# Optimization experiments

Measured on AMD Instinct MI355X. Metric: run time of the kernel, lower is better.

Reference implementation:

```python
import jax, jax.numpy as jnp
import numpy as np

GRID_SIZE = 5
SPLINE_ORDER = 3
TY = 16  # n_ahead


def b_splines(x, grid):
    # x: (B, in), grid: (in, grid_size + 2*spline_order + 1) -> (B, in, grid_size+spline_order)
    x = x[..., None]
    bases = ((x >= grid[:, :-1]) & (x < grid[:, 1:])).astype(x.dtype)
    for k in range(1, SPLINE_ORDER + 1):
        bases = ((x - grid[:, :-(k + 1)]) / (grid[:, k:-1] - grid[:, :-(k + 1)]) * bases[..., :-1]
                 + (grid[:, k + 1:] - x) / (grid[:, k + 1:] - grid[:, 1:-k]) * bases[..., 1:])
    return bases


def kan_linear(x, grid, base_weight, spline_weight, spline_scaler):
    # efficient-kan KANLinear: SiLU base branch + scaled spline branch
    base = jnp.dot(jax.nn.silu(x), base_weight.T)                  # (B, out)
    scaled_sw = spline_weight * spline_scaler[..., None]            # (out, in, coeff)
    spl = jnp.einsum('big,oig->bo', b_splines(x, grid), scaled_sw)
    return base + spl


def setup_inputs() -> dict:
    key = jax.random.key(0)
    ks = jax.random.split(key, 8)
    B, Tx, IN0, H, OUT = 1024, 64, 256, 512, 1
    coeff = GRID_SIZE + SPLINE_ORDER
    x = jax.random.normal(ks[0], (B, Tx, IN0), dtype=jnp.float32)
    h0 = jnp.zeros((B, H), dtype=jnp.float32)
    hstep = 2.0 / GRID_SIZE  # grid_range [-1, 1]
    grid1d = jnp.arange(-SPLINE_ORDER, GRID_SIZE + SPLINE_ORDER + 1, dtype=jnp.float32) * hstep - 1.0
    grid = jnp.broadcast_to(grid1d, (IN0, grid1d.shape[0])).astype(jnp.float32)
    base_weight = jax.random.normal(ks[1], (H, IN0), jnp.float32) * (1.0 / np.sqrt(IN0))
    spline_weight = jax.random.normal(ks[2], (H, IN0, coeff), jnp.float32) * 0.1
    spline_scaler = jax.random.normal(ks[3], (H, IN0), jnp.float32) * (1.0 / np.sqrt(IN0))
    h2h_w = jax.random.normal(ks[4], (H, H), jnp.float32) * (1.0 / np.sqrt(H))
    h2h_b = jnp.zeros((H,), jnp.float32)
    fc_w = jax.random.normal(ks[5], (OUT, H), jnp.float32) * (1.0 / np.sqrt(H))
    fc_b = jnp.zeros((OUT,), jnp.float32)
    return {"x": x, "h0": h0, "grid": grid, "base_weight": base_weight,
            "spline_weight": spline_weight, "spline_scaler": spline_scaler,
            "h2h_w": h2h_w, "h2h_b": h2h_b, "fc_w": fc_w, "fc_b": fc_b}


def reference(x, h0, grid, base_weight, spline_weight, spline_scaler, h2h_w, h2h_b, fc_w, fc_b):
    B, Tx, IN0 = x.shape

    def enc_step(h, x_t):
        h_new = jnp.tanh(kan_linear(x_t, grid, base_weight, spline_weight, spline_scaler)
                         + jnp.dot(h, h2h_w.T) + h2h_b)
        return h_new, h_new

    h_last, h_enc = jax.lax.scan(enc_step, h0, jnp.swapaxes(x, 0, 1))  # h_enc: (Tx, B, H)

    # decode steps are fed x = zeros, so the KAN input branch is a constant
    i2h_zero = kan_linear(jnp.zeros((B, IN0), x.dtype), grid, base_weight, spline_weight, spline_scaler)

    def dec_step(h, _):
        h_new = jnp.tanh(i2h_zero + jnp.dot(h, h2h_w.T) + h2h_b)
        return h_new, h_new

    _, h_dec = jax.lax.scan(dec_step, h_last, None, length=TY)  # (Ty, B, H)

    h_all = jnp.concatenate([jnp.swapaxes(h_enc, 0, 1), jnp.swapaxes(h_dec, 0, 1)], axis=1)  # (B, Tx+Ty, H)
    y = jnp.dot(h_dec, fc_w.T) + fc_b        # (Ty, B, 1)
    y_pred = jnp.swapaxes(y[..., 0], 0, 1)   # (B, Ty)  == y_pred.squeeze(dim=2)
    return (y_pred, h_all)
```

## Files before the change

kernel.cpp:

```cpp
#include <hip/hip_runtime.h>


using s16x8 = __attribute__((ext_vector_type(8))) short;
using u16x8 = __attribute__((ext_vector_type(8))) unsigned short;
using f32x4 = __attribute__((ext_vector_type(4))) float;
using u32x2 = __attribute__((ext_vector_type(2))) unsigned;

#define HALL_TSTRIDE 512
#define HALL_BSTRIDE (80 * 512)

__device__ __forceinline__ unsigned short f2bf(float f) {
  unsigned u = __builtin_bit_cast(unsigned, f);
  u += 0x7fffu + ((u >> 16) & 1u);
  return (unsigned short)(u >> 16);
}
__device__ __forceinline__ float bf2f(unsigned short h) {
  unsigned u = ((unsigned)h) << 16;
  return __builtin_bit_cast(float, u);
}
__device__ __forceinline__ float silu(float x) {
  return x / (1.f + __expf(-x));
}
__device__ __forceinline__ float tanh_fast(float x) {
  float e2 = __expf(2.f * x);
  return 1.f - 2.f * __builtin_amdgcn_rcpf(e2 + 1.f);
}

__device__ __forceinline__ void basis8_f32(float xv, float g0, float invh, float* out) {
  float u = (xv - g0) * invh;
  float fs = floorf(u);
  int s = (int)fs;
  float r = u - fs;
  float omr = 1.f - r;
  float r2 = r * r, r3 = r2 * r;
  float n0 = (1.f / 6.f) * omr * omr * omr;
  float n1 = (1.f / 6.f) * (3.f * r3 - 6.f * r2 + 4.f);
  float n2 = (1.f / 6.f) * (-3.f * r3 + 3.f * r2 + 3.f * r + 1.f);
  float n3 = (1.f / 6.f) * r3;
#pragma unroll
  for (int j = 0; j < 8; ++j) {
    int d = s - j;
    out[j] = (d == 0) ? n3 : (d == 1) ? n2 : (d == 2) ? n1 : (d == 3) ? n0 : 0.f;
  }
}

__device__ __forceinline__ u16x8 basis8_bf16(float xv, float g0, float invh) {
  float t[8];
  basis8_f32(xv, g0, invh, t);
  u16x8 o;
#pragma unroll
  for (int j = 0; j < 8; ++j) o[j] = f2bf(t[j]);
  return o;
}

__global__ __launch_bounds__(256) void prep_waug2(const float* __restrict__ bw,
                                                  const float* __restrict__ sw,
                                                  const float* __restrict__ sc,
                                                  unsigned short* __restrict__ Waug2) {
  int o = blockIdx.x;
  for (int k = threadIdx.x; k < 2304; k += 256) {
    float v;
    if (k < 256) {
      v = bw[o * 256 + k];
    } else {
      int idx = k - 256;
      int i = idx >> 3, g = idx & 7;
      v = sw[(o * 256 + i) * 8 + g] * sc[o * 256 + i];
    }
    int ks = k >> 6;
    int q = (k >> 3) & 7;
    int p = q ^ (o & 7);
    int e = k & 7;
    Waug2[(long)ks * 32768 + o * 64 + p * 8 + e] = f2bf(v);
  }
}

__global__ __launch_bounds__(256) void prep_whh(const float* __restrict__ w,
                                                unsigned short* __restrict__ hi,
                                                unsigned short* __restrict__ lo) {
  for (int i = blockIdx.x * 256 + threadIdx.x; i < 512 * 512; i += gridDim.x * 256) {
    float v = w[i];
    unsigned short h = f2bf(v);
    hi[i] = h;
    lo[i] = f2bf(v - bf2f(h));
  }
}

__global__ __launch_bounds__(256) void prep_i2hz(const float* __restrict__ sw,
                                                 const float* __restrict__ sc,
                                                 const float* __restrict__ grd,
                                                 float* __restrict__ i2hz,
                                                 unsigned* __restrict__ cnt) {
  __shared__ float red[256];
  const int o = blockIdx.x;
  const int t = threadIdx.x;
  if (o == 0) {
    for (int i = t; i < 64 * 32; i += 256) cnt[i] = 0u;
  }
  float g0 = grd[0];
  float invh = 1.f / (grd[1] - grd[0]);
  float bs[8];
  basis8_f32(0.f, g0, invh, bs);
  const float* swrow = sw + ((long)o * 256 + t) * 8;
  float a = 0.f;
#pragma unroll
  for (int j = 0; j < 8; ++j) a += bs[j] * swrow[j];
  red[t] = a * sc[o * 256 + t];
  __syncthreads();
  for (int w = 128; w > 0; w >>= 1) {
    if (t < w) red[t] += red[t + w];
    __syncthreads();
  }
  if (t == 0) i2hz[o] = red[0];
}

__global__ __launch_bounds__(512, 4) void kan_i2h_gemm(const float* __restrict__ x,
                                                       const float* __restrict__ grd,
                                                       const unsigned short* __restrict__ Waug2,
                                                       float* __restrict__ hall) {
  __shared__ __align__(128) short Bs[256 * 64];
  __shared__ __align__(128) short As[128 * 64];

  const int bid = blockIdx.x;
  const int m0 = (bid >> 1) * 128;
  const int n0 = (bid & 1) * 256;
  const int tid = threadIdx.x;
  const int lane = tid & 63, wave = tid >> 6;
  const int wr = wave >> 2, wc = wave & 3;
  const int colg = lane & 15, kgrp = lane >> 4;

  float g0 = grd[0];
  float invh = 1.f / (grd[1] - grd[0]);

  f32x4 acc[4][4] = {};

  const int arow = tid >> 2, apart = tid & 3;
  const float* xrow = x + (long)(m0 + arow) * 256;
  const int aswz = arow & 7;
  short* const adst0 = (short*)((char*)As + arow * 128 + ((apart * 2) ^ aswz) * 16);
  short* const adst1 = (short*)((char*)As + arow * 128 + ((apart * 2 + 1) ^ aswz) * 16);

  auto computeA = [&](int ks, u16x8& d0, u16x8& d1) {
    int kA = ks * 64 + apart * 16;
    if (ks < 4) {
      const float* xs = xrow + kA;
      f32x4 v0 = *(const f32x4*)(xs);
      f32x4 v1 = *(const f32x4*)(xs + 4);
      f32x4 v2 = *(const f32x4*)(xs + 8);
      f32x4 v3 = *(const f32x4*)(xs + 12);
#pragma unroll
      for (int e = 0; e < 4; ++e) {
        d0[e] = f2bf(silu(v0[e]));
        d0[e + 4] = f2bf(silu(v1[e]));
        d1[e] = f2bf(silu(v2[e]));
        d1[e + 4] = f2bf(silu(v3[e]));
      }
    } else {
      int i0 = (kA - 256) >> 3;
      d0 = basis8_bf16(xrow[i0], g0, invh);
      d1 = basis8_bf16(xrow[i0 + 1], g0, invh);
    }
  };

  u16x8 ar0, ar1;
  computeA(0, ar0, ar1);

  for (int ks = 0; ks < 36; ++ks) {
    {
      const char* bsrc = (const char*)Waug2 + (long)ks * 65536 + n0 * 128 +
                         wave * 4096 + lane * 16;
      char* bdst = (char*)Bs + wave * 4096;
#pragma unroll
      for (int i = 0; i < 4; ++i)
        __builtin_amdgcn_global_load_lds(
            (const __attribute__((address_space(1))) unsigned int*)(bsrc + i * 1024),
            (__attribute__((address_space(3))) unsigned int*)(bdst + i * 1024), 16, 0, 0);
    }
    *(u16x8*)adst0 = ar0;
    *(u16x8*)adst1 = ar1;
    __syncthreads();

    if (ks + 1 < 36) computeA(ks + 1, ar0, ar1);

#pragma unroll
    for (int kk = 0; kk < 2; ++kk) {
      const int q = kk * 4 + kgrp;
      s16x8 a[4], b[4];
#pragma unroll
      for (int i = 0; i < 4; ++i) {
        int ra = wr * 64 + i * 16 + colg;
        a[i] = *(const s16x8*)((const char*)As + ra * 128 + (q ^ (ra & 7)) * 16);
      }
#pragma unroll
      for (int j = 0; j < 4; ++j) {
        int rb = wc * 64 + j * 16 + colg;
        b[j] = *(const s16x8*)((const char*)Bs + rb * 128 + (q ^ (rb & 7)) * 16);
      }
#pragma unroll
      for (int i = 0; i < 4; ++i)
#pragma unroll
        for (int j = 0; j < 4; ++j)
          acc[i][j] = __builtin_amdgcn_mfma_f32_16x16x32_bf16(a[i], b[j], acc[i][j], 0, 0, 0);
    }
    __syncthreads();
  }

  const int c0 = n0 + wc * 64;
#pragma unroll
  for (int i = 0; i < 4; ++i) {
    int mbase = m0 + wr * 64 + i * 16 + (kgrp << 2);
#pragma unroll
    for (int r = 0; r < 4; ++r) {
      int m = mbase + r;
      int bb = m >> 6, tt = m & 63;
      float* orow = hall + (long)bb * HALL_BSTRIDE + (long)tt * HALL_TSTRIDE + c0;
#pragma unroll
      for (int j = 0; j < 4; ++j) orow[j * 16 + colg] = acc[i][j][r];
    }
  }
}

__device__ __forceinline__ void pack_write_h(f32x4 v, int rr, int c16,
                                             char* hHb, char* hLb) {
  unsigned h0 = f2bf(v[0]), h1 = f2bf(v[1]), h2 = f2bf(v[2]), h3 = f2bf(v[3]);
  unsigned l0 = f2bf(v[0] - bf2f((unsigned short)h0));
  unsigned l1 = f2bf(v[1] - bf2f((unsigned short)h1));
  unsigned l2 = f2bf(v[2] - bf2f((unsigned short)h2));
  unsigned l3 = f2bf(v[3] - bf2f((unsigned short)h3));
  u32x2 hw, lw;
  hw[0] = h0 | (h1 << 16); hw[1] = h2 | (h3 << 16);
  lw[0] = l0 | (l1 << 16); lw[1] = l2 | (l3 << 16);
  int byte = (rr * 1024 + c16 * 8) ^ ((rr & 7) << 4);
  *(u32x2*)(hHb + byte) = hw;
  *(u32x2*)(hLb + byte) = lw;
}

__global__ __launch_bounds__(512, 2) void rnn_persist(
    const unsigned short* __restrict__ WhhHi,
    const unsigned short* __restrict__ WhhLo,
    const float* __restrict__ i2hz,
    const float* __restrict__ h2hb,
    const float* __restrict__ h0,
    float* __restrict__ hall,
    unsigned* __restrict__ cnt) {
  __shared__ __align__(16) char hHb[16 * 1024];
  __shared__ __align__(16) char hLb[16 * 1024];

  const int tid = threadIdx.x;
  const int lane = tid & 63;
  const int wave = tid >> 6;
  const int bid = blockIdx.x;
  const int xcd = bid & 7;
  const int j = bid >> 3;
  const int cg = j & 3;
  const int g = xcd * 8 + (j >> 2);
  const int m0 = g * 16;
  const int colg = lane & 15;
  const int kgrp = lane >> 4;
  const int o = cg * 128 + wave * 16 + colg;
  const int aswz = (colg & 7) << 4;

  s16x8 wh[16], wl[16];
#pragma unroll
  for (int kk = 0; kk < 16; ++kk) {
    const unsigned short* ph = WhhHi + (long)o * 512 + kk * 32 + kgrp * 8;
    const unsigned short* pl = WhhLo + (long)o * 512 + kk * 32 + kgrp * 8;
    asm volatile("global_load_dwordx4 %0, %1, off" : "=v"(wh[kk]) : "v"(ph));
    asm volatile("global_load_dwordx4 %0, %1, off" : "=v"(wl[kk]) : "v"(pl));
  }
  const float bias = h2hb[o];
  const float i2z = i2hz[o];
  asm volatile("s_waitcnt vmcnt(0)" ::: "memory");
  __builtin_amdgcn_sched_barrier(0);

  {
    const int rr = tid >> 5, cc = tid & 31;
#pragma unroll
    for (int jj = 0; jj < 4; ++jj) {
      int c16 = cc + jj * 32;
      f32x4 v = *(const f32x4*)(h0 + (long)(m0 + rr) * 512 + c16 * 4);
      pack_write_h(v, rr, c16, hHb, hLb);
    }
  }
  __syncthreads();

  for (int T = 0; T < 80; ++T) {
    float i2v[4];
    if (T < 64) {
#pragma unroll
      for (int r = 0; r < 4; ++r) {
        const float* p = hall + (long)(m0 + kgrp * 4 + r) * HALL_BSTRIDE +
                         (long)T * HALL_TSTRIDE + o;
        asm volatile("global_load_dword %0, %1, off sc0 sc1" : "=v"(i2v[r]) : "v"(p));
      }
    }

    f32x4 aA = {}, aB = {}, aC = {};
#pragma unroll
    for (int kk = 0; kk < 16; ++kk) {
      int abyte = (colg * 1024 + kk * 64 + kgrp * 16) ^ aswz;
      s16x8 ah = *(const s16x8*)(hHb + abyte);
      s16x8 al = *(const s16x8*)(hLb + abyte);
      aA = __builtin_amdgcn_mfma_f32_16x16x32_bf16(ah, wh[kk], aA, 0, 0, 0);
      aB = __builtin_amdgcn_mfma_f32_16x16x32_bf16(ah, wl[kk], aB, 0, 0, 0);
      aC = __builtin_amdgcn_mfma_f32_16x16x32_bf16(al, wh[kk], aC, 0, 0, 0);
    }

    if (T < 64) {
      asm volatile("s_waitcnt vmcnt(0)" ::: "memory");
      __builtin_amdgcn_sched_barrier(0);
    } else {
#pragma unroll
      for (int r = 0; r < 4; ++r) i2v[r] = i2z;
    }

#pragma unroll
    for (int r = 0; r < 4; ++r) {
      float pre = aA[r] + aB[r] + aC[r] + i2v[r] + bias;
      float h = tanh_fast(pre);
      float* p = hall + (long)(m0 + kgrp * 4 + r) * HALL_BSTRIDE +
                 (long)T * HALL_TSTRIDE + o;
      asm volatile("global_store_dword %0, %1, off sc0 sc1" :: "v"(p), "v"(h) : "memory");
    }

    if (T == 79) break;

    asm volatile("s_waitcnt vmcnt(0)" ::: "memory");
    __syncthreads();
    if (tid == 0) {
      __hip_atomic_fetch_add(&cnt[g * 32], 1u, __ATOMIC_RELEASE,
                             __HIP_MEMORY_SCOPE_AGENT);
      unsigned tgt = 4u * (unsigned)(T + 1);
      while (__hip_atomic_load(&cnt[g * 32], __ATOMIC_RELAXED,
                               __HIP_MEMORY_SCOPE_AGENT) < tgt)
        __builtin_amdgcn_s_sleep(2);
    }
    __syncthreads();

    {
      const int rr = tid >> 5, cc = tid & 31;
      const float* src = hall + (long)(m0 + rr) * HALL_BSTRIDE + (long)T * HALL_TSTRIDE;
      f32x4 v[4];
#pragma unroll
      for (int jj = 0; jj < 4; ++jj) {
        const float* p = src + (cc + jj * 32) * 4;
        asm volatile("global_load_dwordx4 %0, %1, off sc0 sc1" : "=v"(v[jj]) : "v"(p));
      }
      asm volatile("s_waitcnt vmcnt(0)" ::: "memory");
      __builtin_amdgcn_sched_barrier(0);
#pragma unroll
      for (int jj = 0; jj < 4; ++jj) pack_write_h(v[jj], rr, cc + jj * 32, hHb, hLb);
    }
    __syncthreads();
  }
}

__global__ __launch_bounds__(256) void y_final(const float* __restrict__ hall,
                                               const float* __restrict__ fcw,
                                               const float* __restrict__ fcb,
                                               float* __restrict__ y) {
  int gw = (blockIdx.x * 256 + threadIdx.x) >> 6;
  int lane = threadIdx.x & 63;
  int bb = gw >> 4, ty = gw & 15;
  const float* hrow = hall + (long)bb * HALL_BSTRIDE + (long)(64 + ty) * HALL_TSTRIDE;
  float s = 0.f;
#pragma unroll
  for (int c = 0; c < 8; ++c) s += hrow[lane + c * 64] * fcw[lane + c * 64];
#pragma unroll
  for (int off = 32; off > 0; off >>= 1) s += __shfl_xor(s, off);
  if (lane == 0) y[bb * 16 + ty] = s + fcb[0];
}

extern "C" void kernel_launch(void* const* d_in, const int* in_sizes, int n_in,
                              void* d_out, int out_size, void* d_ws, size_t ws_size,
                              hipStream_t stream) {
  (void)in_sizes; (void)n_in; (void)out_size; (void)ws_size;
  const float* x   = (const float*)d_in[0];
  const float* h0  = (const float*)d_in[1];
  const float* grd = (const float*)d_in[2];
  const float* bw  = (const float*)d_in[3];
  const float* sw  = (const float*)d_in[4];
  const float* sc  = (const float*)d_in[5];
  const float* whh = (const float*)d_in[6];
  const float* hbb = (const float*)d_in[7];
  const float* fcw = (const float*)d_in[8];
  const float* fcb = (const float*)d_in[9];

  float* out = (float*)d_out;
  float* ypred = out;
  float* hall = out + 1024 * 16;

  char* ws = (char*)d_ws;
  unsigned short* Waug2 = (unsigned short*)(ws);
  unsigned short* WhhHi = (unsigned short*)(ws + 2359296);
  unsigned short* WhhLo = (unsigned short*)(ws + 2883584);
  float*          i2hz  = (float*)(ws + 3407872);
  unsigned*       cnt   = (unsigned*)(ws + 3409920);

  prep_waug2<<<512, 256, 0, stream>>>(bw, sw, sc, Waug2);
  prep_whh<<<512, 256, 0, stream>>>(whh, WhhHi, WhhLo);
  prep_i2hz<<<512, 256, 0, stream>>>(sw, sc, grd, i2hz, cnt);
  kan_i2h_gemm<<<1024, 512, 0, stream>>>(x, grd, Waug2, hall);
  rnn_persist<<<256, 512, 0, stream>>>(WhhHi, WhhLo, i2hz, hbb, h0, hall, cnt);
  y_final<<<4096, 256, 0, stream>>>(hall, fcw, fcb, ypred);
}
```

Baseline: 716.3 us.

## Double-buffer LDS tiles in KAN input GEMM and relax recurrence counter atomic

The i2h GEMM now keeps two LDS buffers for A and B. The next tile's global-to-LDS copy and A-operand compute are issued after the current fragments are read, and before the MFMAs, which removes one barrier per k-step and overlaps loads with math. The cost is double the LDS and launch bounds reduced to 2 blocks per CU. The recurrence kernel's counter increment drops from release to relaxed ordering and relies on the explicit vmcnt wait and sc0/sc1 stores for visibility, which is a memory-ordering risk.

New measurement: 756.6 us. +5.6%, slower.

```diff
diff --git a/kernel.cpp b/kernel.cpp
--- a/kernel.cpp
+++ b/kernel.cpp
@@ -114,12 +114,12 @@
   if (t == 0) i2hz[o] = red[0];
 }
 
-__global__ __launch_bounds__(512, 4) void kan_i2h_gemm(const float* __restrict__ x,
+__global__ __launch_bounds__(512, 2) void kan_i2h_gemm(const float* __restrict__ x,
                                                        const float* __restrict__ grd,
                                                        const unsigned short* __restrict__ Waug2,
                                                        float* __restrict__ hall) {
-  __shared__ __align__(128) short Bs[256 * 64];
-  __shared__ __align__(128) short As[128 * 64];
+  __shared__ __align__(128) short Bs[2][256 * 64];
+  __shared__ __align__(128) short As[2][128 * 64];
 
   const int bid = blockIdx.x;
   const int m0 = (bid >> 1) * 128;
@@ -137,8 +137,8 @@
   const int arow = tid >> 2, apart = tid & 3;
   const float* xrow = x + (long)(m0 + arow) * 256;
   const int aswz = arow & 7;
-  short* const adst0 = (short*)((char*)As + arow * 128 + ((apart * 2) ^ aswz) * 16);
-  short* const adst1 = (short*)((char*)As + arow * 128 + ((apart * 2 + 1) ^ aswz) * 16);
+  const int aoff0 = arow * 128 + ((apart * 2) ^ aswz) * 16;
+  const int aoff1 = arow * 128 + ((apart * 2 + 1) ^ aswz) * 16;
 
   auto computeA = [&](int ks, u16x8& d0, u16x8& d1) {
     int kA = ks * 64 + apart * 16;
@@ -162,47 +162,58 @@
     }
   };
 
+  auto stageB = [&](int ks) {
+    const char* bsrc = (const char*)Waug2 + (long)ks * 65536 + n0 * 128 +
+                       wave * 4096 + lane * 16;
+    char* bdst = (char*)Bs[ks & 1] + wave * 4096;
+#pragma unroll
+    for (int i = 0; i < 4; ++i)
+      __builtin_amdgcn_global_load_lds(
+          (const __attribute__((address_space(1))) unsigned int*)(bsrc + i * 1024),
+          (__attribute__((address_space(3))) unsigned int*)(bdst + i * 1024), 16, 0, 0);
+  };
+
   u16x8 ar0, ar1;
   computeA(0, ar0, ar1);
+  stageB(0);
+  *(u16x8*)((char*)As[0] + aoff0) = ar0;
+  *(u16x8*)((char*)As[0] + aoff1) = ar1;
+  computeA(1, ar0, ar1);
 
   for (int ks = 0; ks < 36; ++ks) {
-    {
-      const char* bsrc = (const char*)Waug2 + (long)ks * 65536 + n0 * 128 +
-                         wave * 4096 + lane * 16;
-      char* bdst = (char*)Bs + wave * 4096;
-#pragma unroll
-      for (int i = 0; i < 4; ++i)
-        __builtin_amdgcn_global_load_lds(
-            (const __attribute__((address_space(1))) unsigned int*)(bsrc + i * 1024),
-            (__attribute__((address_space(3))) unsigned int*)(bdst + i * 1024), 16, 0, 0);
-    }
-    *(u16x8*)adst0 = ar0;
-    *(u16x8*)adst1 = ar1;
     __syncthreads();
-
-    if (ks + 1 < 36) computeA(ks + 1, ar0, ar1);
-
+    const char* asb = (const char*)As[ks & 1];
+    const char* bsb = (const char*)Bs[ks & 1];
+    s16x8 a[2][4], b[2][4];
 #pragma unroll
     for (int kk = 0; kk < 2; ++kk) {
       const int q = kk * 4 + kgrp;
-      s16x8 a[4], b[4];
 #pragma unroll
       for (int i = 0; i < 4; ++i) {
         int ra = wr * 64 + i * 16 + colg;
-        a[i] = *(const s16x8*)((const char*)As + ra * 128 + (q ^ (ra & 7)) * 16);
+        a[kk][i] = *(const s16x8*)(asb + ra * 128 + (q ^ (ra & 7)) * 16);
       }
 #pragma unroll
       for (int j = 0; j < 4; ++j) {
         int rb = wc * 64 + j * 16 + colg;
-        b[j] = *(const s16x8*)((const char*)Bs + rb * 128 + (q ^ (rb & 7)) * 16);
+        b[kk][j] = *(const s16x8*)(bsb + rb * 128 + (q ^ (rb & 7)) * 16);
       }
+    }
+    if (ks + 1 < 36) {
+      stageB(ks + 1);
+      char* asn = (char*)As[(ks + 1) & 1];
+      *(u16x8*)(asn + aoff0) = ar0;
+      *(u16x8*)(asn + aoff1) = ar1;
+      if (ks + 2 < 36) computeA(ks + 2, ar0, ar1);
+    }
+#pragma unroll
+    for (int kk = 0; kk < 2; ++kk)
 #pragma unroll
       for (int i = 0; i < 4; ++i)
 #pragma unroll
         for (int j = 0; j < 4; ++j)
-          acc[i][j] = __builtin_amdgcn_mfma_f32_16x16x32_bf16(a[i], b[j], acc[i][j], 0, 0, 0);
-    }
-    __syncthreads();
+          acc[i][j] = __builtin_amdgcn_mfma_f32_16x16x32_bf16(a[kk][i], b[kk][j],
+                                                              acc[i][j], 0, 0, 0);
   }
 
   const int c0 = n0 + wc * 64;
@@ -328,7 +339,7 @@
     asm volatile("s_waitcnt vmcnt(0)" ::: "memory");
     __syncthreads();
     if (tid == 0) {
-      __hip_atomic_fetch_add(&cnt[g * 32], 1u, __ATOMIC_RELEASE,
+      __hip_atomic_fetch_add(&cnt[g * 32], 1u, __ATOMIC_RELAXED,
                              __HIP_MEMORY_SCOPE_AGENT);
       unsigned tgt = 4u * (unsigned)(T + 1);
       while (__hip_atomic_load(&cnt[g * 32], __ATOMIC_RELAXED,
```
